# Kernel tuning notes

Hardware: AMD Instinct MI355X
Metric: run time of the kernel (lower is better)

## Reference

```python
import jax, jax.numpy as jnp
import numpy as np
import math

HEADS = 3
DH = 128  # per-head out_channels (== output_dim == bdry_dim)
HD = HEADS * DH
E_N, F_N, M_N, P_N, D = 50000, 25000, 100000, 75000, 128


def setup_inputs():
    key = jax.random.key(0)
    ks = jax.random.split(key, 40)
    it = iter(range(40))
    nk = lambda: ks[next(it)]
    h_dE = jax.random.normal(nk(), (E_N, D), jnp.float32)
    h_dF = jax.random.normal(nk(), (F_N, D), jnp.float32)
    e_col = jax.random.randint(nk(), (M_N,), 0, E_N)
    f_col = jax.random.randint(nk(), (M_N,), 0, F_N)
    sgn = 2 * jax.random.randint(nk(), (M_N,), 0, 2) - 1  # +/-1 orientation
    cobdry_idx = jnp.stack([e_col, f_col, sgn], axis=1)
    nn_idx = jnp.stack([jax.random.randint(nk(), (P_N,), 0, F_N),
                        jax.random.randint(nk(), (P_N,), 0, F_N),
                        jax.random.randint(nk(), (P_N,), 0, E_N)], axis=1)
    g = lambda shape, fan: jax.random.normal(nk(), shape, jnp.float32) / math.sqrt(fan)
    return dict(
        h_dE=h_dE, h_dF=h_dF, cobdry_idx=cobdry_idx, nn_idx=nn_idx,
        aggr_W=g((D, D), D), aggr_b=jnp.zeros((D,), jnp.float32),
        ctr_W=g((D, D), D), ctr_b=jnp.zeros((D,), jnp.float32),
        f_Wq=g((3, D, HD), D), f_bq=jnp.zeros((3, HD), jnp.float32),
        f_Wk=g((3, D, HD), D), f_bk=jnp.zeros((3, HD), jnp.float32),
        f_Wv=g((3, D, HD), D), f_bv=jnp.zeros((3, HD), jnp.float32),
        f_We=g((3, D, HD), D),
        f_Ws=g((3, D, D), D), f_bs=jnp.zeros((3, D), jnp.float32),
        e_Wq=g((D, HD), D), e_bq=jnp.zeros((HD,), jnp.float32),
        e_Wk=g((D, HD), D), e_bk=jnp.zeros((HD,), jnp.float32),
        e_Wv=g((D, HD), D), e_bv=jnp.zeros((HD,), jnp.float32),
        e_We=g((D, HD), D),
        e_Ws=g((D, D), D), e_bs=jnp.zeros((D,), jnp.float32))


def _seg_softmax(alpha, idx, n):
    # PyG-style segment softmax over destination nodes
    amax = jax.ops.segment_max(alpha, idx, num_segments=n)
    amax = jnp.where(jnp.isfinite(amax), amax, 0.0)
    ex = jnp.exp(alpha - amax[idx])
    den = jax.ops.segment_sum(ex, idx, num_segments=n)
    return ex / (den[idx] + 1e-16)


def _tconv(x_src, x_dst, src, dst, eattr, Wq, bq, Wk, bk, Wv, bv, We, Ws, bs):
    # PyG TransformerConv, heads=HEADS, concat=False, root_weight=True, edge_dim set
    n_dst = x_dst.shape[0]
    q = (x_dst @ Wq + bq).reshape(n_dst, HEADS, DH)
    k = (x_src @ Wk + bk).reshape(-1, HEADS, DH)
    v = (x_src @ Wv + bv).reshape(-1, HEADS, DH)
    e = (eattr @ We).reshape(-1, HEADS, DH)  # lin_edge has bias=False
    kj = k[src] + e
    vj = v[src] + e
    alpha = (q[dst] * kj).sum(-1) / math.sqrt(DH)            # [n_edges, heads]
    alpha = _seg_softmax(alpha, dst, n_dst)
    out = jax.ops.segment_sum(alpha[..., None] * vj, dst, num_segments=n_dst)
    return out.mean(axis=1) + (x_dst @ Ws + bs)              # head mean + root skip


def reference(h_dE, h_dF, cobdry_idx, nn_idx, aggr_W, aggr_b, ctr_W, ctr_b,
              f_Wq, f_bq, f_Wk, f_bk, f_Wv, f_bv, f_We, f_Ws, f_bs,
              e_Wq, e_bq, e_Wk, e_bk, e_Wv, e_bv, e_We, e_Ws, e_bs):
    F_n = h_dF.shape[0]
    sgn = cobdry_idx[:, 2:].astype(h_dE.dtype)               # [M,1] +/-1
    # scatter-add aggregation of signed edge features onto faces
    h_aggr = jax.ops.segment_sum(h_dE[cobdry_idx[:, 0]] * sgn,
                                 cobdry_idx[:, 1], num_segments=F_n)
    h = (h_aggr @ aggr_W + aggr_b) + (h_dF @ ctr_W + ctr_b)
    src, dst = nn_idx[:, 0], nn_idx[:, 1]
    ea = h_dE[nn_idx[:, 2]]
    for l in range(3):  # 3 face transformer layers with residual
        h = _tconv(h, h, src, dst, ea,
                   f_Wq[l], f_bq[l], f_Wk[l], f_bk[l], f_Wv[l], f_bv[l],
                   f_We[l], f_Ws[l], f_bs[l]) + h
    # edge update: in the original, faces are offset by E in a concat; sources are
    # always faces and targets always edges, so this is exactly face->edge attention.
    e_attr = h[cobdry_idx[:, 1]] * sgn
    return _tconv(h, h_dE, cobdry_idx[:, 1], cobdry_idx[:, 0], e_attr,
                  e_Wq, e_bq, e_Wk, e_bk, e_Wv, e_bv, e_We, e_Ws, e_bs)
```

## Files before the change

### kernel.cpp

```cpp
#include <hip/hip_runtime.h>
#include <math.h>

#define E_Nc 50000
#define F_Nc 25000
#define M_Nc 100000
#define P_Nc 75000

typedef unsigned short ushort;
typedef unsigned int uint;
typedef __attribute__((ext_vector_type(8))) short short8v;
typedef __attribute__((ext_vector_type(4))) float float4v;

static inline int cdiv(long a, long b) { return (int)((a + b - 1) / b); }

__device__ inline ushort f2b(float f) {
    uint u = __float_as_uint(f);
    u += 0x7fffu + ((u >> 16) & 1u);
    return (ushort)(u >> 16);
}
__device__ inline float b2f(ushort b) { return __uint_as_float((uint)b << 16); }

__device__ inline int xcd_swz(int bid, int nb) {
    int q = nb >> 3, r = nb & 7;
    int xcd = bid & 7, w = bid >> 3;
    return (xcd < r ? xcd * (q + 1) : r * (q + 1) + (xcd - r) * q) + w;
}

__device__ inline float rsum32(float v) {
    v += __uint_as_float(__builtin_amdgcn_update_dpp(
        0, __float_as_uint(v), 0xB1, 0xF, 0xF, true));
    v += __uint_as_float(__builtin_amdgcn_update_dpp(
        0, __float_as_uint(v), 0x4E, 0xF, 0xF, true));
    v += __uint_as_float(__builtin_amdgcn_update_dpp(
        0, __float_as_uint(v), 0x124, 0xF, 0xF, true));
    v += __uint_as_float(__builtin_amdgcn_update_dpp(
        0, __float_as_uint(v), 0x128, 0xF, 0xF, true));
    v += __shfl_xor(v, 16);
    return v;
}

__global__ void zero_f(float* __restrict__ p, int n) {
    int i = blockIdx.x * blockDim.x + threadIdx.x;
    if (i < n) p[i] = 0.f;
}

struct CsrJob {
    const int* idx3;
    int col, srccol, P, n;
    int* cnt;
    int* rp;
    int2* epack;
    int* bsum;
};
struct CsrJobs { CsrJob j[3]; };

__global__ __launch_bounds__(256) void csr_zero(CsrJobs js) {
    const CsrJob& j = js.j[blockIdx.y];
    int i = blockIdx.x * 256 + threadIdx.x;
    if (i < j.n) j.cnt[i] = 0;
}

__global__ __launch_bounds__(256) void csr_count(CsrJobs js) {
    const CsrJob& j = js.j[blockIdx.y];
    int i = blockIdx.x * 256 + threadIdx.x;
    if (i < j.P) atomicAdd(&j.cnt[j.idx3[(size_t)i * 3 + j.col]], 1);
}

__global__ __launch_bounds__(256) void csr_scan_partial(CsrJobs js) {
    const CsrJob& j = js.j[blockIdx.y];
    __shared__ int lds[256];
    int b = blockIdx.x, t = threadIdx.x;
    int base = b * 1024 + t * 4;
    int s = 0;
    #pragma unroll
    for (int k = 0; k < 4; k++) { int i = base + k; if (i < j.n) s += j.cnt[i]; }
    lds[t] = s;
    __syncthreads();
    for (int off = 128; off > 0; off >>= 1) {
        if (t < off) lds[t] += lds[t + off];
        __syncthreads();
    }
    if (t == 0) j.bsum[b] = lds[0];
}

__global__ __launch_bounds__(64) void csr_scan_bsum(CsrJobs js) {
    const CsrJob& j = js.j[blockIdx.y];
    __shared__ int lds[64];
    int t = threadIdx.x;
    int v = j.bsum[t];
    lds[t] = v;
    __syncthreads();
    for (int off = 1; off < 64; off <<= 1) {
        int x = (t >= off) ? lds[t - off] : 0;
        __syncthreads();
        lds[t] += x;
        __syncthreads();
    }
    j.bsum[t] = lds[t] - v;
}

__global__ __launch_bounds__(256) void csr_scan_final(CsrJobs js) {
    const CsrJob& j = js.j[blockIdx.y];
    __shared__ int lds[256];
    int b = blockIdx.x, t = threadIdx.x;
    int base = b * 1024 + t * 4;
    int v[4];
    int s = 0;
    #pragma unroll
    for (int k = 0; k < 4; k++) {
        int i = base + k;
        v[k] = (i < j.n) ? j.cnt[i] : 0;
        s += v[k];
    }
    lds[t] = s;
    __syncthreads();
    for (int off = 1; off < 256; off <<= 1) {
        int x = (t >= off) ? lds[t - off] : 0;
        __syncthreads();
        lds[t] += x;
        __syncthreads();
    }
    int pre = j.bsum[b] + lds[t] - s;
    #pragma unroll
    for (int k = 0; k < 4; k++) {
        int i = base + k;
        if (i < j.n) j.rp[i] = pre;
        pre += v[k];
        if (i == j.n - 1) j.rp[j.n] = pre;
    }
}

__global__ __launch_bounds__(256) void csr_scatter(CsrJobs js) {
    const CsrJob& j = js.j[blockIdx.y];
    int i = blockIdx.x * 256 + threadIdx.x;
    if (i >= j.P) return;
    const int* row = j.idx3 + (size_t)i * 3;
    int d = row[j.col];
    int pos = atomicAdd(&j.cnt[d], 1);
    int2 pk;
    pk.x = row[j.srccol];
    pk.y = row[2];
    j.epack[j.rp[d] + pos] = pk;
}

struct GuArgs { const float* wq[4]; const float* we[4]; const float* wk[4]; };
__global__ __launch_bounds__(256) void compute_gu(GuArgs a,
        float* __restrict__ Wu32, float* __restrict__ G32) {
    int idx = blockIdx.x * 256 + threadIdx.x;
    if (idx >= 2 * 12 * 16384) return;
    int sel = idx / (12 * 16384);
    int rem0 = idx - sel * (12 * 16384);
    int lh = rem0 >> 14;
    int l = lh / 3, h = lh - l * 3;
    int rem = rem0 & 16383;
    int c = rem >> 7, d = rem & 127;
    const float* Wq = a.wq[l];
    const float* Wo = sel ? a.wk[l] : a.we[l];
    float s = 0.f;
    #pragma unroll 4
    for (int jj = 0; jj < 128; jj++)
        s += Wq[d * 384 + h * 128 + jj] * Wo[c * 384 + h * 128 + jj];
    (sel ? G32 : Wu32)[rem0] = s;
}

struct WkbArgs { const float* wk[4]; const float* bq[4]; };
__global__ void wkb_k(WkbArgs a, float* __restrict__ wkb32) {
    int idx = blockIdx.x * blockDim.x + threadIdx.x;
    if (idx >= 4 * 384) return;
    int l = idx / 384;
    int r = idx - l * 384;
    int h = r >> 7, d = r & 127;
    const float* Wk = a.wk[l];
    const float* bq = a.bq[l];
    float s = 0.f;
    for (int jj = 0; jj < 128; jj++)
        s += Wk[d * 384 + h * 128 + jj] * bq[h * 128 + jj];
    wkb32[idx] = s;
}

struct BvArgs { const float* bv[4]; };
__global__ void bvmean_k(BvArgs a, float* __restrict__ pool) {
    int idx = blockIdx.x * blockDim.x + threadIdx.x;
    if (idx >= 4 * 128) return;
    int l = idx >> 7, c = idx & 127;
    float v = (a.bv[l][c] + a.bv[l][128 + c] + a.bv[l][256 + c]) * (1.f / 3.f);
    pool[(l < 3 ? 3840 + l * 128 : 4224) + c] = v;
}

struct BuArgs { const float* bq[4]; const float* we[4]; };
__global__ void bias_u(BuArgs a, float* __restrict__ pool) {
    int idx = blockIdx.x * blockDim.x + threadIdx.x;
    if (idx >= 12 * 128) return;
    int lh = idx >> 7, c = idx & 127;
    int l = lh / 3, h = lh - l * 3;
    const float* bq = a.bq[l];
    const float* We = a.we[l];
    float s = 0.f;
    for (int jj = 0; jj < 128; jj++)
        s += bq[h * 128 + jj] * We[c * 384 + h * 128 + jj];
    int slot = (l < 3) ? (l * 960 + 384 + h * 128 + c)
                       : (2880 + 384 + h * 128 + c);
    pool[slot] = s;
}

struct BDesc { const float* src; int dstoff, n; };
struct BDescs { BDesc d[8]; };
__global__ void copy_bias(BDescs ds, float* __restrict__ pool) {
    const BDesc b = ds.d[blockIdx.y];
    int i = blockIdx.x * 256 + threadIdx.x;
    if (i < b.n) pool[b.dstoff + i] = b.src[i];
}

struct WDesc {
    const float* in;
    long outoff;
    int ldin, coloff, NN, KK, trans, ldo;
};
struct WDescs { WDesc d[44]; int cnt; };

__global__ __launch_bounds__(256) void prep_weights(WDescs ds, ushort* __restrict__ out) {
    const WDesc w = ds.d[blockIdx.y];
    int i = blockIdx.x * 256 + threadIdx.x;
    if (i >= w.NN * w.KK) return;
    int n = i / w.KK, k = i - n * w.KK;
    float v = w.trans ? w.in[(size_t)k * w.ldin + w.coloff + n]
                      : w.in[(size_t)n * w.ldin + w.coloff + k];
    ushort hi = f2b(v);
    ushort lo = f2b(v - b2f(hi));
    long ro = w.outoff + (size_t)n * w.ldo;
    out[ro + k] = hi;
    out[ro + w.KK + k] = lo;
}

__global__ __launch_bounds__(256) void cob_gather(
        const float* __restrict__ h_dE, const int2* __restrict__ epack,
        const int* __restrict__ rp, float* __restrict__ out, int Fn) {
    int wave = (int)((blockIdx.x * (size_t)blockDim.x + threadIdx.x) >> 6);
    int lane = threadIdx.x & 63;
    if (wave >= Fn) return;
    float2 s = make_float2(0.f, 0.f);
    int beg = rp[wave], end = rp[wave + 1];
    for (int e = beg; e < end; e++) {
        int2 sp = epack[e];
        float sg = (float)sp.y;
        float2 v = *(const float2*)(h_dE + (size_t)sp.x * 128 + lane * 2);
        s.x += sg * v.x;
        s.y += sg * v.y;
    }
    *(float2*)(out + (size_t)wave * 128 + lane * 2) = s;
}

#define TPB 3
struct SegInfo {
    float* base[5];
    int ld[5];
    int start[6];
    int nseg;
};

__global__ __launch_bounds__(256) void gemm_xproj(
        const float* __restrict__ A, int lda, int M,
        const ushort* __restrict__ Wt,
        const float* __restrict__ biasAll,
        SegInfo segs, int nys) {
    __shared__ ushort LDSu[64][264];
    const int j = xcd_swz(blockIdx.x, gridDim.x);
    const int ys = j % nys;
    const int bm = (j / nys) * 64;
    const int t = threadIdx.x;
    const int lane = t & 63;
    const int wv = t >> 6;
    #pragma unroll
    for (int i = 0; i < 8; i++) {
        int li = t + i * 256;
        int r = li >> 5, q4 = li & 31;
        int m = bm + r;
        float4 v = make_float4(0.f, 0.f, 0.f, 0.f);
        if (m < M) v = *(const float4*)(A + (size_t)m * lda + q4 * 4);
        ushort h0 = f2b(v.x), h1 = f2b(v.y), h2 = f2b(v.z), h3 = f2b(v.w);
        ushort l0 = f2b(v.x - b2f(h0)), l1 = f2b(v.y - b2f(h1));
        ushort l2 = f2b(v.z - b2f(h2)), l3 = f2b(v.w - b2f(h3));
        *(uint2*)&LDSu[r][q4 * 4] =
            make_uint2((uint)h0 | ((uint)h1 << 16), (uint)h2 | ((uint)h3 << 16));
        *(uint2*)&LDSu[r][128 + q4 * 4] =
            make_uint2((uint)l0 | ((uint)l1 << 16), (uint)l2 | ((uint)l3 << 16));
    }
    __syncthreads();
    const int arow = wv * 16 + (lane & 15);
    const int kb = (lane >> 4) * 8;
    const int bcol = lane & 15;
    short8v a_hi[4], a_lo[4];
    #pragma unroll
    for (int kc = 0; kc < 4; kc++) {
        a_hi[kc] = *(const short8v*)&LDSu[arow][kc * 32 + kb];
        a_lo[kc] = *(const short8v*)&LDSu[arow][128 + kc * 32 + kb];
    }
    const int Ntot = segs.start[segs.nseg];
    const int bn0 = ys * (TPB * 64);
    const int bn1 = min(bn0 + TPB * 64, Ntot);
    if (bn0 >= Ntot) return;
    short8v breg[8];
    #pragma unroll
    for (int i = 0; i < 8; i++) {
        int li = t + i * 256;
        int r = li >> 5, g = li & 31;
        breg[i] = *(const short8v*)(Wt + (size_t)(bn0 + r) * 256 + g * 8);
    }
    int seg = 0;
    while (bn0 >= segs.start[seg + 1]) seg++;
    for (int bn = bn0; bn < bn1; bn += 64) {
        while (bn >= segs.start[seg + 1]) seg++;
        __syncthreads();
        #pragma unroll
        for (int i = 0; i < 8; i++) {
            int li = t + i * 256;
            int r = li >> 5, g = li & 31;
            *(short8v*)&LDSu[r][g * 8] = breg[i];
        }
        __syncthreads();
        if (bn + 64 < bn1) {
            #pragma unroll
            for (int i = 0; i < 8; i++) {
                int li = t + i * 256;
                int r = li >> 5, g = li & 31;
                breg[i] = *(const short8v*)(Wt + (size_t)(bn + 64 + r) * 256 + g * 8);
            }
        }
        float4v acc[4] = {{0.f, 0.f, 0.f, 0.f}, {0.f, 0.f, 0.f, 0.f},
                          {0.f, 0.f, 0.f, 0.f}, {0.f, 0.f, 0.f, 0.f}};
        #pragma unroll
        for (int kc = 0; kc < 4; kc++) {
            #pragma unroll
            for (int f = 0; f < 4; f++) {
                short8v bh = *(const short8v*)&LDSu[f * 16 + bcol][kc * 32 + kb];
                short8v bl = *(const short8v*)&LDSu[f * 16 + bcol][128 + kc * 32 + kb];
                acc[f] = __builtin_amdgcn_mfma_f32_16x16x32_bf16(a_hi[kc], bh, acc[f], 0, 0, 0);
                acc[f] = __builtin_amdgcn_mfma_f32_16x16x32_bf16(a_lo[kc], bh, acc[f], 0, 0, 0);
                acc[f] = __builtin_amdgcn_mfma_f32_16x16x32_bf16(a_hi[kc], bl, acc[f], 0, 0, 0);
            }
        }
        float* Cb = segs.base[seg];
        const int ldc = segs.ld[seg];
        const int coff = segs.start[seg];
        const int rb = bm + wv * 16 + ((lane >> 4) << 2);
        #pragma unroll
        for (int f = 0; f < 4; f++) {
            int ng = bn + f * 16 + bcol;
            float bias = biasAll[ng];
            int col = ng - coff;
            #pragma unroll
            for (int r = 0; r < 4; r++) {
                int row = rb + r;
                if (row < M && col < ldc)
                    Cb[(size_t)row * ldc + col] = acc[f][r] + bias;
            }
        }
    }
}

template <int OUTM, bool HASBIAS>
__global__ __launch_bounds__(256) void gemm_split(
        const float* __restrict__ A, int lda,
        const ushort* __restrict__ Wt, int ldw,
        const float* __restrict__ bias,
        float* __restrict__ C, int ldc,
        int M, int N, int kper) {
    __shared__ ushort Bs[64][264];
    const int koff = blockIdx.z * kper;
    const int bm = blockIdx.x * 64;
    const int bn = blockIdx.y * 64;
    const int t = threadIdx.x;
    const int lane = t & 63;
    const int wv = t >> 6;
    const int arow = wv * 16 + (lane & 15);
    const int kb = (lane >> 4) * 8;
    const int bcol = lane & 15;
    const int m = bm + arow;
    const bool mok = (m < M);
    const float* Arow = A + (size_t)m * lda + koff + kb;
    float4v acc[4] = {{0.f, 0.f, 0.f, 0.f}, {0.f, 0.f, 0.f, 0.f},
                      {0.f, 0.f, 0.f, 0.f}, {0.f, 0.f, 0.f, 0.f}};
    short8v breg[8];
    #pragma unroll
    for (int i = 0; i < 8; i++) {
        int li = t + i * 256;
        int r = li >> 5, g = li & 31;
        breg[i] = *(const short8v*)(Wt + (size_t)(bn + r) * ldw + (koff >> 7) * 256 + g * 8);
    }
    for (int c = 0; c < kper; c += 128) {
        __syncthreads();
        #pragma unroll
        for (int i = 0; i < 8; i++) {
            int li = t + i * 256;
            int r = li >> 5, g = li & 31;
            *(short8v*)&Bs[r][g * 8] = breg[i];
        }
        __syncthreads();
        if (c + 128 < kper) {
            const int nchunk = (koff + c + 128) >> 7;
            #pragma unroll
            for (int i = 0; i < 8; i++) {
                int li = t + i * 256;
                int r = li >> 5, g = li & 31;
                breg[i] = *(const short8v*)(Wt + (size_t)(bn + r) * ldw + nchunk * 256 + g * 8);
            }
        }
        short8v a_hi[4], a_lo[4];
        #pragma unroll
        for (int kc = 0; kc < 4; kc++) {
            float4 v0 = make_float4(0.f, 0.f, 0.f, 0.f);
            float4 v1 = make_float4(0.f, 0.f, 0.f, 0.f);
            if (mok) {
                v0 = *(const float4*)(Arow + c + kc * 32);
                v1 = *(const float4*)(Arow + c + kc * 32 + 4);
            }
            union { short8v v; ushort u[8]; } hi, lo;
            float vv[8] = {v0.x, v0.y, v0.z, v0.w, v1.x, v1.y, v1.z, v1.w};
            #pragma unroll
            for (int jj = 0; jj < 8; jj++) {
                ushort hj = f2b(vv[jj]);
                hi.u[jj] = hj;
                lo.u[jj] = f2b(vv[jj] - b2f(hj));
            }
            a_hi[kc] = hi.v;
            a_lo[kc] = lo.v;
        }
        #pragma unroll
        for (int kc = 0; kc < 4; kc++) {
            #pragma unroll
            for (int f = 0; f < 4; f++) {
                short8v bh = *(const short8v*)&Bs[f * 16 + bcol][kc * 32 + kb];
                short8v bl = *(const short8v*)&Bs[f * 16 + bcol][128 + kc * 32 + kb];
                acc[f] = __builtin_amdgcn_mfma_f32_16x16x32_bf16(a_hi[kc], bh, acc[f], 0, 0, 0);
                acc[f] = __builtin_amdgcn_mfma_f32_16x16x32_bf16(a_lo[kc], bh, acc[f], 0, 0, 0);
                acc[f] = __builtin_amdgcn_mfma_f32_16x16x32_bf16(a_hi[kc], bl, acc[f], 0, 0, 0);
            }
        }
    }
    const int rb = bm + wv * 16 + ((lane >> 4) << 2);
    #pragma unroll
    for (int f = 0; f < 4; f++) {
        int col = bn + f * 16 + bcol;
        #pragma unroll
        for (int r = 0; r < 4; r++) {
            int row = rb + r;
            if (row >= M) continue;
            float val = acc[f][r];
            if (HASBIAS) val += bias[col];
            size_t idx = (size_t)row * ldc + col;
            if (OUTM == 0) {
                C[idx] = val;
            } else if (OUTM == 1) {
                C[idx] += val;
            } else {
                atomicAdd(&C[idx], val);
            }
        }
    }
}

template <bool HASSEED>
__global__ __launch_bounds__(256) void gemm_yz(
        const ushort* __restrict__ A,
        const ushort* __restrict__ Wt,
        const float* __restrict__ seed,
        float* __restrict__ out,
        const int* __restrict__ rp,
        const float* __restrict__ bvm, int M) {
    __shared__ ushort Bs[64][264];
    const int j = xcd_swz(blockIdx.x, gridDim.x);
    const int by = j & 1;
    const int bm = (j >> 1) * 64;
    const int bn = by * 64;
    const int t = threadIdx.x;
    const int lane = t & 63;
    const int wv = t >> 6;
    const int arow = wv * 16 + (lane & 15);
    const int kb = (lane >> 4) * 8;
    const int bcol = lane & 15;
    const int m = bm + arow;
    const bool mok = (m < M);
    const ushort* Ar = A + (size_t)m * 1536 + kb;
    const short8v z8 = {0, 0, 0, 0, 0, 0, 0, 0};
    short8v breg[8];
    #pragma unroll
    for (int i = 0; i < 8; i++) {
        int li = t + i * 256;
        int r = li >> 5, g = li & 31;
        breg[i] = *(const short8v*)(Wt + (size_t)(bn + r) * 1536 + g * 8);
    }
    short8v aH[2][4], aL[2][4];
    #pragma unroll
    for (int kc = 0; kc < 4; kc++) {
        aH[0][kc] = mok ? *(const short8v*)(Ar + kc * 32) : z8;
        aL[0][kc] = mok ? *(const short8v*)(Ar + 768 + kc * 32) : z8;
    }
    float4v acc[4] = {{0.f, 0.f, 0.f, 0.f}, {0.f, 0.f, 0.f, 0.f},
                      {0.f, 0.f, 0.f, 0.f}, {0.f, 0.f, 0.f, 0.f}};
    #pragma unroll
    for (int c = 0; c < 6; c++) {
        const int cur = c & 1, nxt = cur ^ 1;
        __syncthreads();
        #pragma unroll
        for (int i = 0; i < 8; i++) {
            int li = t + i * 256;
            int r = li >> 5, g = li & 31;
            *(short8v*)&Bs[r][g * 8] = breg[i];
        }
        __syncthreads();
        if (c < 5) {
            #pragma unroll
            for (int i = 0; i < 8; i++) {
                int li = t + i * 256;
                int r = li >> 5, g = li & 31;
                breg[i] = *(const short8v*)(Wt + (size_t)(bn + r) * 1536 + (c + 1) * 256 + g * 8);
            }
            #pragma unroll
            for (int kc = 0; kc < 4; kc++) {
                aH[nxt][kc] = mok ? *(const short8v*)(Ar + (c + 1) * 128 + kc * 32) : z8;
                aL[nxt][kc] = mok ? *(const short8v*)(Ar + 768 + (c + 1) * 128 + kc * 32) : z8;
            }
        }
        #pragma unroll
        for (int kc = 0; kc < 4; kc++) {
            short8v ah = aH[cur][kc];
            short8v al = aL[cur][kc];
            #pragma unroll
            for (int f = 0; f < 4; f++) {
                short8v bh = *(const short8v*)&Bs[f * 16 + bcol][kc * 32 + kb];
                short8v bl = *(const short8v*)&Bs[f * 16 + bcol][128 + kc * 32 + kb];
                acc[f] = __builtin_amdgcn_mfma_f32_16x16x32_bf16(ah, bh, acc[f], 0, 0, 0);
                acc[f] = __builtin_amdgcn_mfma_f32_16x16x32_bf16(al, bh, acc[f], 0, 0, 0);
                acc[f] = __builtin_amdgcn_mfma_f32_16x16x32_bf16(ah, bl, acc[f], 0, 0, 0);
            }
        }
    }
    const int rb = bm + wv * 16 + ((lane >> 4) << 2);
    float ind[4];
    #pragma unroll
    for (int r = 0; r < 4; r++) {
        int row = rb + r;
        ind[r] = (row < M && rp[row + 1] > rp[row]) ? 1.f : 0.f;
    }
    #pragma unroll
    for (int f = 0; f < 4; f++) {
        int col = bn + f * 16 + bcol;
        float bv = bvm[col];
        #pragma unroll
        for (int r = 0; r < 4; r++) {
            int row = rb + r;
            if (row >= M) continue;
            size_t idx = (size_t)row * 128 + col;
            float val = acc[f][r] + ind[r] * bv;
            if (HASSEED) val += seed[idx];
            out[idx] += val;
        }
    }
}

template <int EMODE>
__global__ __launch_bounds__(256) void attn_fused(
        const float* __restrict__ A1, const float* __restrict__ U,
        const float* __restrict__ X, const float* __restrict__ Esrc,
        const float* __restrict__ kvec, const int2* __restrict__ epack,
        const int* __restrict__ rp,
        ushort* __restrict__ YZ, int n_dst) {
    int dst = (int)((blockIdx.x * (size_t)blockDim.x + threadIdx.x) >> 5);
    int lane = threadIdx.x & 31;
    if (dst >= n_dst) return;
    const float* ap = A1 + (size_t)dst * 384;
    const float* up = U + (size_t)dst * 384;
    float4 a1[3], u[3], y[3], za[3];
    float m[3], den[3];
    #pragma unroll
    for (int h = 0; h < 3; h++) {
        a1[h] = *(const float4*)(ap + h * 128 + lane * 4);
        u[h] = *(const float4*)(up + h * 128 + lane * 4);
        y[h] = make_float4(0.f, 0.f, 0.f, 0.f);
        za[h] = make_float4(0.f, 0.f, 0.f, 0.f);
        m[h] = -INFINITY;
        den[h] = 0.f;
    }
    int beg = rp[dst], end = rp[dst + 1];
    auto loadE = [&](int e, float4& xs, float4& ea, float4& kv) {
        int2 sp = epack[e];
        xs = *(const float4*)(X + (size_t)sp.x * 128 + lane * 4);
        if (EMODE == 0) {
            ea = *(const float4*)(Esrc + (size_t)sp.y * 128 + lane * 4);
        } else {
            float sgn = (float)sp.y;
            ea = make_float4(xs.x * sgn, xs.y * sgn, xs.z * sgn, xs.w * sgn);
        }
        kv = *(const float4*)(kvec + (size_t)sp.x * 4);
    };
    float4 xA, eA, kA, xB, eB, kB;
    if (beg < end) loadE(beg, xA, eA, kA);
    if (beg + 1 < end) loadE(beg + 1, xB, eB, kB);
    for (int e = beg; e < end; e++) {
        float4 xC, eC, kC;
        if (e + 2 < end) loadE(e + 2, xC, eC, kC);
        float dot[3];
        #pragma unroll
        for (int h = 0; h < 3; h++)
            dot[h] = a1[h].x * xA.x + a1[h].y * xA.y +
                     a1[h].z * xA.z + a1[h].w * xA.w +
                     u[h].x * eA.x + u[h].y * eA.y +
                     u[h].z * eA.z + u[h].w * eA.w;
        #pragma unroll
        for (int h = 0; h < 3; h++) dot[h] = rsum32(dot[h]);
        float kvh[3] = {kA.x, kA.y, kA.z};
        #pragma unroll
        for (int h = 0; h < 3; h++) {
            float a = (dot[h] + kvh[h]) * 0.08838834764831845f;
            float mn = fmaxf(m[h], a);
            float scale = __expf(m[h] - mn);
            float w = __expf(a - mn);
            den[h] = den[h] * scale + w;
            y[h].x = y[h].x * scale + w * xA.x;
            y[h].y = y[h].y * scale + w * xA.y;
            y[h].z = y[h].z * scale + w * xA.z;
            y[h].w = y[h].w * scale + w * xA.w;
            za[h].x = za[h].x * scale + w * eA.x;
            za[h].y = za[h].y * scale + w * eA.y;
            za[h].z = za[h].z * scale + w * eA.z;
            za[h].w = za[h].w * scale + w * eA.w;
            m[h] = mn;
        }
        xA = xB; eA = eB; kA = kB;
        xB = xC; eB = eC; kB = kC;
    }
    ushort* yrow = YZ + (size_t)dst * 1536;
    #pragma unroll
    for (int h = 0; h < 3; h++) {
        float inv = 1.f / (den[h] + 1e-16f) * (1.f / 3.f);
        float vy[4] = {y[h].x * inv, y[h].y * inv, y[h].z * inv, y[h].w * inv};
        float vz[4] = {za[h].x * inv, za[h].y * inv, za[h].z * inv, za[h].w * inv};
        ushort hy[4], ly[4], hz[4], lz[4];
        #pragma unroll
        for (int jj = 0; jj < 4; jj++) {
            hy[jj] = f2b(vy[jj]);
            ly[jj] = f2b(vy[jj] - b2f(hy[jj]));
            hz[jj] = f2b(vz[jj]);
            lz[jj] = f2b(vz[jj] - b2f(hz[jj]));
        }
        *(uint2*)(yrow + h * 128 + lane * 4) =
            make_uint2((uint)hy[0] | ((uint)hy[1] << 16), (uint)hy[2] | ((uint)hy[3] << 16));
        *(uint2*)(yrow + 768 + h * 128 + lane * 4) =
            make_uint2((uint)ly[0] | ((uint)ly[1] << 16), (uint)ly[2] | ((uint)ly[3] << 16));
        *(uint2*)(yrow + 384 + h * 128 + lane * 4) =
            make_uint2((uint)hz[0] | ((uint)hz[1] << 16), (uint)hz[2] | ((uint)hz[3] << 16));
        *(uint2*)(yrow + 768 + 384 + h * 128 + lane * 4) =
            make_uint2((uint)lz[0] | ((uint)lz[1] << 16), (uint)lz[2] | ((uint)lz[3] << 16));
    }
}

extern "C" void kernel_launch(void* const* d_in, const int* in_sizes, int n_in,
                              void* d_out, int out_size, void* d_ws, size_t ws_size,
                              hipStream_t stream) {
    const float* h_dE  = (const float*)d_in[0];
    const float* h_dF  = (const float*)d_in[1];
    const int*   cob   = (const int*)d_in[2];
    const int*   nn    = (const int*)d_in[3];
    const float* aggrW = (const float*)d_in[4];
    const float* aggrB = (const float*)d_in[5];
    const float* ctrW  = (const float*)d_in[6];
    const float* ctrB  = (const float*)d_in[7];
    const float* f_Wq  = (const float*)d_in[8];
    const float* f_bq  = (const float*)d_in[9];
    const float* f_Wk  = (const float*)d_in[10];
    const float* f_bk  = (const float*)d_in[11];
    const float* f_Wv  = (const float*)d_in[12];
    const float* f_bv  = (const float*)d_in[13];
    const float* f_We  = (const float*)d_in[14];
    const float* f_Ws  = (const float*)d_in[15];
    const float* f_bs  = (const float*)d_in[16];
    const float* e_Wq  = (const float*)d_in[17];
    const float* e_bq  = (const float*)d_in[18];
    const float* e_Wk  = (const float*)d_in[19];
    const float* e_bk  = (const float*)d_in[20];
    const float* e_Wv  = (const float*)d_in[21];
    const float* e_bv  = (const float*)d_in[22];
    const float* e_We  = (const float*)d_in[23];
    const float* e_Ws  = (const float*)d_in[24];
    const float* e_bs  = (const float*)d_in[25];

    const int CH = 25000;

    char* base = (char*)d_ws;
    size_t off = 0;
    auto takeB = [&](size_t bytes) {
        char* p = base + off;
        off += (bytes + 15) & ~(size_t)15;
        return p;
    };
    float*  h     = (float*)takeB((size_t)F_Nc * 128 * 4);
    float*  A1f   = (float*)takeB((size_t)CH * 384 * 4);
    float*  Uf    = (float*)takeB((size_t)CH * 384 * 4);
    float*  YZb   = (float*)takeB((size_t)CH * 768 * 4);
    float*  Kvb   = (float*)takeB((size_t)CH * 4 * 4);
    float*  Wu32  = (float*)takeB((size_t)12 * 16384 * 4);
    float*  G32   = (float*)takeB((size_t)12 * 16384 * 4);
    float*  wkb32 = (float*)takeB((size_t)4 * 384 * 4);
    float*  biasPool = (float*)takeB(4608 * 4);
    ushort* WtPool = (ushort*)takeB((size_t)2200000 * 2);
    int* rp_nn   = (int*)takeB((F_Nc + 1) * 4);
    int* rp_cobE = (int*)takeB((E_Nc + 1) * 4);
    int* rp_cobF = (int*)takeB((F_Nc + 1) * 4);
    int2* epk_nn = (int2*)takeB((size_t)P_Nc * 8);
    int2* epk_cE = (int2*)takeB((size_t)M_Nc * 8);
    int2* epk_cF = (int2*)takeB((size_t)M_Nc * 8);
    int* cnt_nn  = (int*)takeB((size_t)F_Nc * 4);
    int* cnt_cE  = (int*)takeB((size_t)E_Nc * 4);
    int* cnt_cF  = (int*)takeB((size_t)F_Nc * 4);
    int* bsum3   = (int*)takeB(3 * 64 * 4);
    if (ws_size < off) return;

    const int BLK = 256;
    float* dout = (float*)d_out;
    ushort* YZu = (ushort*)YZb;

    const float* Wq4[4] = {f_Wq, f_Wq + 49152, f_Wq + 98304, e_Wq};
    const float* Wk4[4] = {f_Wk, f_Wk + 49152, f_Wk + 98304, e_Wk};
    const float* Wv4[4] = {f_Wv, f_Wv + 49152, f_Wv + 98304, e_Wv};
    const float* We4[4] = {f_We, f_We + 49152, f_We + 98304, e_We};
    const float* Ws4[4] = {f_Ws, f_Ws + 16384, f_Ws + 32768, e_Ws};
    const float* bq4[4] = {f_bq, f_bq + 384, f_bq + 768, e_bq};
    const float* bv4[4] = {f_bv, f_bv + 384, f_bv + 768, e_bv};

    zero_f<<<cdiv(4608, BLK), BLK, 0, stream>>>(biasPool, 4608);
    GuArgs gua;
    BuArgs bua;
    WkbArgs wka;
    BvArgs bva;
    for (int l = 0; l < 4; l++) {
        gua.wq[l] = Wq4[l]; gua.we[l] = We4[l]; gua.wk[l] = Wk4[l];
        bua.bq[l] = bq4[l]; bua.we[l] = We4[l];
        wka.wk[l] = Wk4[l]; wka.bq[l] = bq4[l];
        bva.bv[l] = bv4[l];
    }
    compute_gu<<<cdiv(2 * 12 * 16384, BLK), BLK, 0, stream>>>(gua, Wu32, G32);
    bias_u<<<cdiv(12 * 128, BLK), BLK, 0, stream>>>(bua, biasPool);
    wkb_k<<<cdiv(4 * 384, BLK), BLK, 0, stream>>>(wka, wkb32);
    bvmean_k<<<cdiv(4 * 128, BLK), BLK, 0, stream>>>(bva, biasPool);

    BDescs bd;
    int bi = 0;
    auto addb = [&](const float* s, int o, int n2) { bd.d[bi].src = s; bd.d[bi].dstoff = o; bd.d[bi].n = n2; bi++; };
    for (int l = 0; l < 3; l++) addb(f_bs + l * 128, l * 960 + 832, 128);
    addb(e_bs, 2880 + 768, 128);
    copy_bias<<<dim3(1, 4), BLK, 0, stream>>>(bd, biasPool);

    WDescs wd;
    int dc = 0;
    long wto = 0;
    auto addw = [&](const float* in, int ldin, int coloff, long outoff,
                    int NN, int KK, int trans, int ldo) {
        wd.d[dc].in = in; wd.d[dc].ldin = ldin; wd.d[dc].coloff = coloff;
        wd.d[dc].outoff = outoff; wd.d[dc].NN = NN; wd.d[dc].KK = KK;
        wd.d[dc].trans = trans; wd.d[dc].ldo = ldo; dc++;
    };
    long wx[3], w4e, w4h, wyz[4], waggr, wctr;
    for (int l = 0; l < 3; l++) {
        wx[l] = wto;
        addw(G32 + (long)l * 49152, 128, 0, wto, 384, 128, 0, 256);
        addw(Wu32 + (long)l * 49152, 128, 0, wto + 384L * 256, 384, 128, 0, 256);
        addw(wkb32 + (long)l * 384, 128, 0, wto + 768L * 256, 3, 128, 0, 256);
        addw(Ws4[l], 128, 0, wto + 832L * 256, 128, 128, 1, 256);
        wto += 960L * 256;
    }
    w4e = wto;
    addw(G32 + 3L * 49152, 128, 0, wto, 384, 128, 0, 256);
    addw(Wu32 + 3L * 49152, 128, 0, wto + 384L * 256, 384, 128, 0, 256);
    addw(e_Ws, 128, 0, wto + 768L * 256, 128, 128, 1, 256);
    wto += 896L * 256;
    w4h = wto;
    addw(wkb32 + 3L * 384, 128, 0, wto, 3, 128, 0, 256);
    wto += 64L * 256;
    for (int l = 0; l < 4; l++) {
        wyz[l] = wto;
        for (int hh = 0; hh < 3; hh++) {
            addw(Wv4[l], 384, hh * 128, wto + hh * 256, 128, 128, 1, 1536);
            addw(We4[l], 384, hh * 128, wto + (3 + hh) * 256, 128, 128, 1, 1536);
        }
        wto += 128L * 1536;
    }
    waggr = wto; addw(aggrW, 128, 0, wto, 128, 128, 1, 256); wto += 128 * 256;
    wctr  = wto; addw(ctrW,  128, 0, wto, 128, 128, 1, 256); wto += 128 * 256;
    wd.cnt = dc;
    prep_weights<<<dim3(192, dc), BLK, 0, stream>>>(wd, WtPool);

    CsrJobs cj;
    cj.j[0] = {nn, 1, 0, P_Nc, F_Nc, cnt_nn, rp_nn, epk_nn, bsum3};
    cj.j[1] = {cob, 0, 1, M_Nc, E_Nc, cnt_cE, rp_cobE, epk_cE, bsum3 + 64};
    cj.j[2] = {cob, 1, 0, M_Nc, F_Nc, cnt_cF, rp_cobF, epk_cF, bsum3 + 128};
    csr_zero<<<dim3(cdiv(E_Nc, BLK), 3), BLK, 0, stream>>>(cj);
    csr_count<<<dim3(cdiv(M_Nc, BLK), 3), BLK, 0, stream>>>(cj);
    csr_scan_partial<<<dim3(cdiv(E_Nc, 1024), 3), BLK, 0, stream>>>(cj);
    csr_scan_bsum<<<dim3(1, 3), 64, 0, stream>>>(cj);
    csr_scan_final<<<dim3(cdiv(E_Nc, 1024), 3), BLK, 0, stream>>>(cj);
    csr_zero<<<dim3(cdiv(E_Nc, BLK), 3), BLK, 0, stream>>>(cj);
    csr_scatter<<<dim3(cdiv(M_Nc, BLK), 3), BLK, 0, stream>>>(cj);

    cob_gather<<<cdiv((long)F_Nc * 64, BLK), BLK, 0, stream>>>(
        h_dE, epk_cF, rp_cobF, YZb, F_Nc);

    gemm_split<0, true><<<dim3(cdiv(F_Nc, 64), 2, 1), BLK, 0, stream>>>(
        YZb, 128, WtPool + waggr, 256, aggrB, h, 128, F_Nc, 128, 128);
    gemm_split<1, true><<<dim3(cdiv(F_Nc, 64), 2, 1), BLK, 0, stream>>>(
        h_dF, 128, WtPool + wctr, 256, ctrB, h, 128, F_Nc, 128, 128);

    const int NXB = cdiv(F_Nc, 64);

    for (int l = 0; l < 3; l++) {
        SegInfo s3;
        s3.base[0] = A1f; s3.ld[0] = 384;
        s3.base[1] = Uf;  s3.ld[1] = 384;
        s3.base[2] = Kvb; s3.ld[2] = 4;
        s3.base[3] = dout; s3.ld[3] = 128;
        s3.base[4] = nullptr; s3.ld[4] = 0;
        s3.start[0] = 0; s3.start[1] = 384; s3.start[2] = 768;
        s3.start[3] = 832; s3.start[4] = 960; s3.start[5] = 960;
        s3.nseg = 4;
        gemm_xproj<<<dim3(NXB * 5), BLK, 0, stream>>>(
            h, 128, F_Nc, WtPool + wx[l], biasPool + l * 960, s3, 5);
        attn_fused<0><<<cdiv((long)F_Nc * 32, BLK), BLK, 0, stream>>>(
            A1f, Uf, h, h_dE, Kvb, epk_nn, rp_nn, YZu, F_Nc);
        gemm_yz<true><<<dim3(NXB * 2), BLK, 0, stream>>>(
            YZu, WtPool + wyz[l], dout, h, rp_nn,
            biasPool + 3840 + l * 128, F_Nc);
    }

    {
        SegInfo s4h;
        s4h.base[0] = Kvb; s4h.ld[0] = 4;
        s4h.base[1] = nullptr; s4h.base[2] = nullptr; s4h.base[3] = nullptr; s4h.base[4] = nullptr;
        s4h.ld[1] = 0; s4h.ld[2] = 0; s4h.ld[3] = 0; s4h.ld[4] = 0;
        s4h.start[0] = 0; s4h.start[1] = 64; s4h.start[2] = 64;
        s4h.start[3] = 64; s4h.start[4] = 64; s4h.start[5] = 64;
        s4h.nseg = 1;
        gemm_xproj<<<dim3(NXB), BLK, 0, stream>>>(
            h, 128, F_Nc, WtPool + w4h, biasPool + 3776, s4h, 1);
    }
    for (int c = 0; c < 2; c++) {
        int c0 = c * CH;
        SegInfo s4e;
        s4e.base[0] = A1f; s4e.ld[0] = 384;
        s4e.base[1] = Uf;  s4e.ld[1] = 384;
        s4e.base[2] = dout + (size_t)c0 * 128; s4e.ld[2] = 128;
        s4e.base[3] = nullptr; s4e.base[4] = nullptr; s4e.ld[3] = 0; s4e.ld[4] = 0;
        s4e.start[0] = 0; s4e.start[1] = 384; s4e.start[2] = 768;
        s4e.start[3] = 896; s4e.start[4] = 896; s4e.start[5] = 896;
        s4e.nseg = 3;
        gemm_xproj<<<dim3(cdiv(CH, 64) * 5), BLK, 0, stream>>>(
            h_dE + (size_t)c0 * 128, 128, CH, WtPool + w4e, biasPool + 2880, s4e, 5);
        attn_fused<1><<<cdiv((long)CH * 32, BLK), BLK, 0, stream>>>(
            A1f, Uf, h, h, Kvb, epk_cE, rp_cobE + c0, YZu, CH);
        gemm_yz<false><<<dim3(cdiv(CH, 64) * 2), BLK, 0, stream>>>(
            YZu, WtPool + wyz[3], nullptr, dout + (size_t)c0 * 128, rp_cobE + c0,
            biasPool + 4224, CH);
    }
}
```

Measured before the change: 746.3 us.

## Drop LDS staging in gemm_yz and shrink N tile to 32 columns

The gemm_yz kernel no longer stages weight tiles through shared memory with block barriers. Each lane now loads its B fragments directly from global memory, which should hit L2 or cache since the weights are small. The output tile per block is narrowed from 64 to 32 columns and the grid doubled, trading more re-reads of the A rows for more blocks and no synchronisation. Each wave redundantly reads the same weights, and the A matrix (1536-wide bf16 rows) is now streamed four times instead of twice.

```diff
diff --git a/kernel.cpp b/kernel.cpp
--- a/kernel.cpp
+++ b/kernel.cpp
@@ -467,11 +467,10 @@
         float* __restrict__ out,
         const int* __restrict__ rp,
         const float* __restrict__ bvm, int M) {
-    __shared__ ushort Bs[64][264];
     const int j = xcd_swz(blockIdx.x, gridDim.x);
-    const int by = j & 1;
-    const int bm = (j >> 1) * 64;
-    const int bn = by * 64;
+    const int by = j & 3;
+    const int bm = (j >> 2) * 64;
+    const int bn = by * 32;
     const int t = threadIdx.x;
     const int lane = t & 63;
     const int wv = t >> 6;
@@ -481,40 +480,19 @@
     const int m = bm + arow;
     const bool mok = (m < M);
     const ushort* Ar = A + (size_t)m * 1536 + kb;
+    const ushort* Wb = Wt + (size_t)(bn + bcol) * 1536 + kb;
     const short8v z8 = {0, 0, 0, 0, 0, 0, 0, 0};
-    short8v breg[8];
-    #pragma unroll
-    for (int i = 0; i < 8; i++) {
-        int li = t + i * 256;
-        int r = li >> 5, g = li & 31;
-        breg[i] = *(const short8v*)(Wt + (size_t)(bn + r) * 1536 + g * 8);
-    }
     short8v aH[2][4], aL[2][4];
     #pragma unroll
     for (int kc = 0; kc < 4; kc++) {
         aH[0][kc] = mok ? *(const short8v*)(Ar + kc * 32) : z8;
         aL[0][kc] = mok ? *(const short8v*)(Ar + 768 + kc * 32) : z8;
     }
-    float4v acc[4] = {{0.f, 0.f, 0.f, 0.f}, {0.f, 0.f, 0.f, 0.f},
-                      {0.f, 0.f, 0.f, 0.f}, {0.f, 0.f, 0.f, 0.f}};
+    float4v acc[2] = {{0.f, 0.f, 0.f, 0.f}, {0.f, 0.f, 0.f, 0.f}};
     #pragma unroll
     for (int c = 0; c < 6; c++) {
         const int cur = c & 1, nxt = cur ^ 1;
-        __syncthreads();
-        #pragma unroll
-        for (int i = 0; i < 8; i++) {
-            int li = t + i * 256;
-            int r = li >> 5, g = li & 31;
-            *(short8v*)&Bs[r][g * 8] = breg[i];
-        }
-        __syncthreads();
         if (c < 5) {
-            #pragma unroll
-            for (int i = 0; i < 8; i++) {
-                int li = t + i * 256;
-                int r = li >> 5, g = li & 31;
-                breg[i] = *(const short8v*)(Wt + (size_t)(bn + r) * 1536 + (c + 1) * 256 + g * 8);
-            }
             #pragma unroll
             for (int kc = 0; kc < 4; kc++) {
                 aH[nxt][kc] = mok ? *(const short8v*)(Ar + (c + 1) * 128 + kc * 32) : z8;
@@ -523,16 +501,18 @@
         }
         #pragma unroll
         for (int kc = 0; kc < 4; kc++) {
+            short8v bh0 = *(const short8v*)(Wb + c * 256 + kc * 32);
+            short8v bl0 = *(const short8v*)(Wb + c * 256 + kc * 32 + 128);
+            short8v bh1 = *(const short8v*)(Wb + 16 * 1536 + c * 256 + kc * 32);
+            short8v bl1 = *(const short8v*)(Wb + 16 * 1536 + c * 256 + kc * 32 + 128);
             short8v ah = aH[cur][kc];
             short8v al = aL[cur][kc];
-            #pragma unroll
-            for (int f = 0; f < 4; f++) {
-                short8v bh = *(const short8v*)&Bs[f * 16 + bcol][kc * 32 + kb];
-                short8v bl = *(const short8v*)&Bs[f * 16 + bcol][128 + kc * 32 + kb];
-                acc[f] = __builtin_amdgcn_mfma_f32_16x16x32_bf16(ah, bh, acc[f], 0, 0, 0);
-                acc[f] = __builtin_amdgcn_mfma_f32_16x16x32_bf16(al, bh, acc[f], 0, 0, 0);
-                acc[f] = __builtin_amdgcn_mfma_f32_16x16x32_bf16(ah, bl, acc[f], 0, 0, 0);
-            }
+            acc[0] = __builtin_amdgcn_mfma_f32_16x16x32_bf16(ah, bh0, acc[0], 0, 0, 0);
+            acc[0] = __builtin_amdgcn_mfma_f32_16x16x32_bf16(al, bh0, acc[0], 0, 0, 0);
+            acc[0] = __builtin_amdgcn_mfma_f32_16x16x32_bf16(ah, bl0, acc[0], 0, 0, 0);
+            acc[1] = __builtin_amdgcn_mfma_f32_16x16x32_bf16(ah, bh1, acc[1], 0, 0, 0);
+            acc[1] = __builtin_amdgcn_mfma_f32_16x16x32_bf16(al, bh1, acc[1], 0, 0, 0);
+            acc[1] = __builtin_amdgcn_mfma_f32_16x16x32_bf16(ah, bl1, acc[1], 0, 0, 0);
         }
     }
     const int rb = bm + wv * 16 + ((lane >> 4) << 2);
@@ -543,7 +523,7 @@
         ind[r] = (row < M && rp[row + 1] > rp[row]) ? 1.f : 0.f;
     }
     #pragma unroll
-    for (int f = 0; f < 4; f++) {
+    for (int f = 0; f < 2; f++) {
         int col = bn + f * 16 + bcol;
         float bv = bvm[col];
         #pragma unroll
@@ -825,7 +805,7 @@
             h, 128, F_Nc, WtPool + wx[l], biasPool + l * 960, s3, 5);
         attn_fused<0><<<cdiv((long)F_Nc * 32, BLK), BLK, 0, stream>>>(
             A1f, Uf, h, h_dE, Kvb, epk_nn, rp_nn, YZu, F_Nc);
-        gemm_yz<true><<<dim3(NXB * 2), BLK, 0, stream>>>(
+        gemm_yz<true><<<dim3(NXB * 4), BLK, 0, stream>>>(
             YZu, WtPool + wyz[l], dout, h, rp_nn,
             biasPool + 3840 + l * 128, F_Nc);
     }
@@ -855,7 +835,7 @@
             h_dE + (size_t)c0 * 128, 128, CH, WtPool + w4e, biasPool + 2880, s4e, 5);
         attn_fused<1><<<cdiv((long)CH * 32, BLK), BLK, 0, stream>>>(
             A1f, Uf, h, h, Kvb, epk_cE, rp_cobE + c0, YZu, CH);
-        gemm_yz<false><<<dim3(cdiv(CH, 64) * 2), BLK, 0, stream>>>(
+        gemm_yz<false><<<dim3(cdiv(CH, 64) * 4), BLK, 0, stream>>>(
             YZu, WtPool + wyz[3], nullptr, dout + (size_t)c0 * 128, rp_cobE + c0,
             biasPool + 4224, CH);
     }
```

Result: slower. 1.105 ms (+48.1%).
